# Kernel optimization log

Measured on AMD Instinct MI355X. Metric: run time of the kernel, lower is better.

## Reference

```python
import jax, jax.numpy as jnp
import numpy as np

EPSILON = 8.0        # Gibbs kernel temperature (JCPOTConfig.epsilon)
NUM_INNER_ITER = 10  # Sinkhorn u/v fixed-point iterations
STAB = 1e-8          # denominator stabilizer, matches torch code


def _cost_matrix(s, t):
    # Euclidean pairwise distance, same math as torch.norm(s[:,None]-t[None,:], dim=2)
    # computed without materializing the [n_s, n_t, d] tensor.
    sq = jnp.sum(s * s, axis=1)[:, None] + jnp.sum(t * t, axis=1)[None, :] - 2.0 * (s @ t.T)
    return jnp.sqrt(jnp.maximum(sq, 0.0))


def setup_inputs() -> dict:
    key = jax.random.key(0)
    k1, k2 = jax.random.split(key)
    return {
        "source_features": jax.random.normal(k1, (4096, 512), dtype=jnp.float32),
        "target_features": jax.random.normal(k2, (4096, 512), dtype=jnp.float32),
    }


def reference(source_features, target_features):
    n_s = source_features.shape[0]
    n_t = target_features.shape[0]
    C = _cost_matrix(source_features, target_features)   # [n_s, n_t]
    K = jnp.exp(-C / EPSILON)                             # Gibbs kernel

    # uniform marginals (JCPOT passes uniform weights; Sinkhorn renormalizes -> same)
    a = jnp.full((n_s, 1), 1.0 / n_s, dtype=C.dtype)
    b = jnp.full((n_t, 1), 1.0 / n_t, dtype=C.dtype)

    def body(carry, _):
        u, v = carry
        u = a / (K @ v + STAB)
        v = b / (K.T @ u + STAB)
        return (u, v), None

    u0 = jnp.ones((n_s, 1), dtype=C.dtype)
    v0 = jnp.ones((n_t, 1), dtype=C.dtype)
    (u, v), _ = jax.lax.scan(body, (u0, v0), None, length=NUM_INNER_ITER)

    coupling = u * K * v.T                                # [n_s, n_t]
    ot_loss = jnp.sum(coupling * C) / (n_s * n_t)         # reduction='mean'
    # returns same contents as the torch dict: ot_loss, coupling, cost_matrix
    return ot_loss, coupling, C
```

## Files before the change

kernel.cpp:

```cpp
#include <hip/hip_runtime.h>
#include <math.h>


#define N_S 4096
#define N_T 4096
#define DIM 512
#define STAB 1e-8f

typedef _Float16 f16x4 __attribute__((ext_vector_type(4)));
typedef _Float16 f16x8 __attribute__((ext_vector_type(8)));
typedef float f32x4v __attribute__((ext_vector_type(4)));

#define SINK_BLOCKS 1024

__global__ __launch_bounds__(256) void k_norms(const float4* __restrict__ S4,
                                               const float4* __restrict__ T4,
                                               float* __restrict__ ns, float* __restrict__ nt) {
    int t = threadIdx.x;
    int lane = t & 63, wave = t >> 6;
    int wid = blockIdx.x * 4 + wave;
    const float4* src; float* dst; int row;
    if (wid < N_S) { src = S4; dst = ns; row = wid; }
    else           { src = T4; dst = nt; row = wid - N_S; }
    float acc = 0.f;
#pragma unroll
    for (int c = 0; c < 2; ++c) {
        float4 x = src[row * 128 + c * 64 + lane];
        acc += x.x*x.x + x.y*x.y + x.z*x.z + x.w*x.w;
    }
#pragma unroll
    for (int m = 32; m; m >>= 1) acc += __shfl_xor(acc, m);
    if (lane == 0) dst[row] = acc;
}

__global__ __launch_bounds__(256) void k_cvt(const float* __restrict__ S, const float* __restrict__ T,
                                             _Float16* __restrict__ Sh2, _Float16* __restrict__ Th2) {
    int g = blockIdx.x * 256 + threadIdx.x;
    const float* src; _Float16* dst;
    if (g < 262144) { src = S; dst = Sh2; }
    else            { src = T; dst = Th2; g -= 262144; }
    int row = g >> 6, cb = (g & 63) * 8;
    float4 x0 = *(const float4*)(src + (size_t)row * 512 + cb);
    float4 x1 = *(const float4*)(src + (size_t)row * 512 + cb + 4);
    f16x8 h = { (_Float16)x0.x, (_Float16)x0.y, (_Float16)x0.z, (_Float16)x0.w,
                (_Float16)x1.x, (_Float16)x1.y, (_Float16)x1.z, (_Float16)x1.w };
    *(f16x8*)(dst + ((size_t)(cb >> 5) * 4096 + row) * 32 + (cb & 31)) = h;
}

__global__ void k_init(float* v, float* vacc, double* lossd) {
    int g = blockIdx.x * 256 + threadIdx.x;
    if (g < N_T) { v[g] = 1.0f; vacc[g] = 0.0f; }
    if (g == 0) *lossd = 0.0;
}

__global__ __launch_bounds__(256) void k_gemm16(const _Float16* __restrict__ Sh2,
                                                const _Float16* __restrict__ Th2,
                                                const float* __restrict__ ns,
                                                const float* __restrict__ nt,
                                                float* __restrict__ outC) {
    __shared__ _Float16 As[128 * 40];
    __shared__ _Float16 Bs[128 * 40];
    int t = threadIdx.x;
    int lane = t & 63, wave = t >> 6;
    int wr = wave >> 1, wc = wave & 1;
    int brow = blockIdx.x * 128, bcol = blockIdx.y * 128;

    f32x4v acc[4][4] = {};

    for (int kt = 0; kt < 16; ++kt) {
        __syncthreads();
        const _Float16* Ab = Sh2 + ((size_t)kt * 4096 + brow) * 32;
        const _Float16* Bb = Th2 + ((size_t)kt * 4096 + bcol) * 32;
#pragma unroll
        for (int w = 0; w < 2; ++w) {
            int e = w * 2048 + t * 8, row = e >> 5, col = e & 31;
            *(f16x8*)(&As[row * 40 + col]) = *(const f16x8*)(Ab + row * 32 + col);
            *(f16x8*)(&Bs[row * 40 + col]) = *(const f16x8*)(Bb + row * 32 + col);
        }
        __syncthreads();

        f16x8 af[4], bf[4];
#pragma unroll
        for (int m = 0; m < 4; ++m)
            af[m] = *(const f16x8*)(&As[(wr * 64 + m * 16 + (lane & 15)) * 40 + (lane >> 4) * 8]);
#pragma unroll
        for (int n = 0; n < 4; ++n)
            bf[n] = *(const f16x8*)(&Bs[(wc * 64 + n * 16 + (lane & 15)) * 40 + (lane >> 4) * 8]);
#pragma unroll
        for (int m = 0; m < 4; ++m)
#pragma unroll
            for (int n = 0; n < 4; ++n)
                acc[m][n] = __builtin_amdgcn_mfma_f32_16x16x32_f16(af[m], bf[n], acc[m][n], 0, 0, 0);
    }

#pragma unroll
    for (int m = 0; m < 4; ++m) {
#pragma unroll
        for (int n = 0; n < 4; ++n) {
#pragma unroll
            for (int r = 0; r < 4; ++r) {
                int i = brow + wr * 64 + m * 16 + (lane >> 4) * 4 + r;
                int j = bcol + wc * 64 + n * 16 + (lane & 15);
                float sq = ns[i] + nt[j] - 2.0f * acc[m][n][r];
                outC[(size_t)i * N_T + j] = sqrtf(fmaxf(sq, 0.0f));
            }
        }
    }
}

__global__ __launch_bounds__(256) void k_kh(const float* __restrict__ Cd, _Float16* __restrict__ Kh) {
    size_t i = ((size_t)blockIdx.x * 256 + threadIdx.x) * 8;
    float4 c0 = *(const float4*)(Cd + i);
    float4 c1 = *(const float4*)(Cd + i + 4);
    f16x8 h;
    h[0] = (_Float16)__expf(c0.x * -0.125f);
    h[1] = (_Float16)__expf(c0.y * -0.125f);
    h[2] = (_Float16)__expf(c0.z * -0.125f);
    h[3] = (_Float16)__expf(c0.w * -0.125f);
    h[4] = (_Float16)__expf(c1.x * -0.125f);
    h[5] = (_Float16)__expf(c1.y * -0.125f);
    h[6] = (_Float16)__expf(c1.z * -0.125f);
    h[7] = (_Float16)__expf(c1.w * -0.125f);
    *(f16x8*)(Kh + i) = h;
}

__global__ __launch_bounds__(256) void k_sink2(const _Float16* __restrict__ Kh,
                                               const float* __restrict__ v,
                                               float* __restrict__ u_out,
                                               float* __restrict__ part) {
    __shared__ _Float16 rows[4][4096];
    __shared__ float u_s[4];
    int t = threadIdx.x, lane = t & 63, w = t >> 6;
    int row = blockIdx.x * 4 + w;
    const _Float16* Kr = Kh + (size_t)row * N_T;

    f16x8 kk[8];
#pragma unroll
    for (int it = 0; it < 8; ++it)
        kk[it] = *(const f16x8*)(Kr + it * 512 + lane * 8);

    float dot = 0.f;
#pragma unroll
    for (int it = 0; it < 8; ++it) {
        int j0 = it * 512 + lane * 8;
        float4 v0 = *(const float4*)(v + j0);
        float4 v1 = *(const float4*)(v + j0 + 4);
        *(f16x8*)(&rows[w][j0]) = kk[it];
        dot += (float)kk[it][0]*v0.x + (float)kk[it][1]*v0.y
             + (float)kk[it][2]*v0.z + (float)kk[it][3]*v0.w
             + (float)kk[it][4]*v1.x + (float)kk[it][5]*v1.y
             + (float)kk[it][6]*v1.z + (float)kk[it][7]*v1.w;
    }
#pragma unroll
    for (int m = 32; m; m >>= 1) dot += __shfl_xor(dot, m);
    if (lane == 0) {
        float uv = (1.0f / N_S) / (dot + STAB);
        u_s[w] = uv;
        u_out[row] = uv;
    }
    __syncthreads();

    float4 acc[4] = {};
#pragma unroll
    for (int s = 0; s < 4; ++s) {
        int jj = t * 4 + s * 1024;
#pragma unroll
        for (int r = 0; r < 4; ++r) {
            f16x4 k4 = *(const f16x4*)(&rows[r][jj]);
            float uu = u_s[r];
            acc[s].x += uu * (float)k4[0];
            acc[s].y += uu * (float)k4[1];
            acc[s].z += uu * (float)k4[2];
            acc[s].w += uu * (float)k4[3];
        }
    }
    float* pb = part + (size_t)blockIdx.x * N_T;
#pragma unroll
    for (int s = 0; s < 4; ++s)
        *(float4*)(pb + t * 4 + s * 1024) = acc[s];
}

__global__ __launch_bounds__(256) void k_vred(const float* __restrict__ part, float* __restrict__ v) {
    __shared__ float sums[256];
    int t = threadIdx.x;
    int c = t & 15, p0 = t >> 4;
    int j = blockIdx.x * 16 + c;
    float acc = 0.f;
#pragma unroll 8
    for (int k = 0; k < 64; ++k)
        acc += part[(size_t)(p0 * 64 + k) * N_T + j];
    sums[t] = acc;
    __syncthreads();
    if (t < 16) {
        float s = 0.f;
#pragma unroll
        for (int c2 = 0; c2 < 16; ++c2) s += sums[c2 * 16 + t];
        v[blockIdx.x * 16 + t] = (1.0f / N_T) / (s + STAB);
    }
}

__global__ __launch_bounds__(256) void k_final3(const _Float16* __restrict__ Kh,
                                                const float* __restrict__ u, const float* __restrict__ v,
                                                float* __restrict__ W, double* __restrict__ lossd) {
    int t = threadIdx.x, row = blockIdx.x;
    float ui = u[row];
    float lacc = 0.f;
    const float NEG8LN2 = -5.5451774444795623f;
    const _Float16* Kr = Kh + (size_t)row * N_T;
    float* Wr = W + (size_t)row * N_T;
#pragma unroll
    for (int cc = 0; cc < 4; ++cc) {
        int j = (cc * 256 + t) * 4;
        f16x4 kk = *(const f16x4*)(Kr + j);
        float4 v4 = *(const float4*)(v + j);
        float4 w4;
        float kf0 = (float)kk[0], kf1 = (float)kk[1], kf2 = (float)kk[2], kf3 = (float)kk[3];
        w4.x = ui * kf0 * v4.x;
        w4.y = ui * kf1 * v4.y;
        w4.z = ui * kf2 * v4.z;
        w4.w = ui * kf3 * v4.w;
        *(float4*)(Wr + j) = w4;
        lacc += w4.x * (NEG8LN2 * __log2f(kf0)) + w4.y * (NEG8LN2 * __log2f(kf1))
              + w4.z * (NEG8LN2 * __log2f(kf2)) + w4.w * (NEG8LN2 * __log2f(kf3));
    }
#pragma unroll
    for (int m = 32; m; m >>= 1) lacc += __shfl_xor(lacc, m);
    __shared__ float wsum[4];
    int lane = t & 63, wave = t >> 6;
    if (lane == 0) wsum[wave] = lacc;
    __syncthreads();
    if (t == 0) atomicAdd(lossd, (double)(wsum[0] + wsum[1] + wsum[2] + wsum[3]));
}

__global__ void k_loss(const double* __restrict__ lossd, float* __restrict__ out0) {
    *out0 = (float)(*lossd / ((double)N_S * (double)N_T));
}

__global__ __launch_bounds__(256) void k_gemm0(const float* __restrict__ S, const float* __restrict__ T,
                                               const float* __restrict__ ns, const float* __restrict__ nt,
                                               float* __restrict__ outK, float* __restrict__ outC) {
    __shared__ _Float16 As[128 * 40];
    __shared__ _Float16 Bs[128 * 40];
    int t = threadIdx.x;
    int lane = t & 63, wave = t >> 6;
    int wr = wave >> 1, wc = wave & 1;
    int brow = blockIdx.x * 128, bcol = blockIdx.y * 128;

    f32x4v acc[4][4] = {};

    for (int kt = 0; kt < DIM; kt += 32) {
        __syncthreads();
#pragma unroll
        for (int w = 0; w < 4; ++w) {
            int e = w * 1024 + t * 4;
            int row = e >> 5, col = e & 31;
            float4 a = *(const float4*)(S + (size_t)(brow + row) * DIM + kt + col);
            f16x4 ah = { (_Float16)a.x, (_Float16)a.y, (_Float16)a.z, (_Float16)a.w };
            *(f16x4*)(&As[row * 40 + col]) = ah;
            float4 b = *(const float4*)(T + (size_t)(bcol + row) * DIM + kt + col);
            f16x4 bh = { (_Float16)b.x, (_Float16)b.y, (_Float16)b.z, (_Float16)b.w };
            *(f16x4*)(&Bs[row * 40 + col]) = bh;
        }
        __syncthreads();

        f16x8 af[4], bf[4];
#pragma unroll
        for (int m = 0; m < 4; ++m)
            af[m] = *(const f16x8*)(&As[(wr * 64 + m * 16 + (lane & 15)) * 40 + (lane >> 4) * 8]);
#pragma unroll
        for (int n = 0; n < 4; ++n)
            bf[n] = *(const f16x8*)(&Bs[(wc * 64 + n * 16 + (lane & 15)) * 40 + (lane >> 4) * 8]);
#pragma unroll
        for (int m = 0; m < 4; ++m)
#pragma unroll
            for (int n = 0; n < 4; ++n)
                acc[m][n] = __builtin_amdgcn_mfma_f32_16x16x32_f16(af[m], bf[n], acc[m][n], 0, 0, 0);
    }

#pragma unroll
    for (int m = 0; m < 4; ++m) {
#pragma unroll
        for (int n = 0; n < 4; ++n) {
#pragma unroll
            for (int r = 0; r < 4; ++r) {
                int i = brow + wr * 64 + m * 16 + (lane >> 4) * 4 + r;
                int j = bcol + wc * 64 + n * 16 + (lane & 15);
                float sq = ns[i] + nt[j] - 2.0f * acc[m][n][r];
                float c = sqrtf(fmaxf(sq, 0.0f));
                size_t idx = (size_t)i * N_T + j;
                outC[idx] = c;
                outK[idx] = __expf(-c * 0.125f);
            }
        }
    }
}

__global__ __launch_bounds__(256) void k_rowmv(const float* __restrict__ Kd,
                                               const float* __restrict__ v, float* __restrict__ u) {
    __shared__ float vl[4096];
    int t = threadIdx.x;
#pragma unroll
    for (int c = 0; c < 16; ++c) vl[c * 256 + t] = v[c * 256 + t];
    __syncthreads();
    int lane = t & 63, wave = t >> 6;
    int row = blockIdx.x * 4 + wave;
    const float* Kr = Kd + (size_t)row * N_T;
    float dot = 0.f;
#pragma unroll 8
    for (int c = 0; c < 64; ++c) {
        int j = c * 64 + lane;
        dot += Kr[j] * vl[j];
    }
#pragma unroll
    for (int m = 32; m; m >>= 1) dot += __shfl_xor(dot, m);
    if (lane == 0) u[row] = (1.0f / N_S) / (dot + STAB);
}

__global__ __launch_bounds__(256) void k_colmv(const float* __restrict__ Kd,
                                               const float* __restrict__ u, float* __restrict__ vacc) {
    __shared__ float ul[64];
    int t = threadIdx.x;
    int rc = blockIdx.y;
    if (t < 64) ul[t] = u[rc * 64 + t];
    __syncthreads();
    int j = blockIdx.x * 256 + t;
    const float* Kp = Kd + (size_t)(rc * 64) * N_T + j;
    float acc = 0.f;
#pragma unroll 8
    for (int r = 0; r < 64; ++r) acc += Kp[(size_t)r * N_T] * ul[r];
    atomicAdd(&vacc[j], acc);
}

__global__ void k_vfin(float* v, float* vacc) {
    int j = blockIdx.x * 256 + threadIdx.x;
    v[j] = (1.0f / N_T) / (vacc[j] + STAB);
    vacc[j] = 0.f;
}

__global__ __launch_bounds__(256) void k_final(float* __restrict__ Kd, const float* __restrict__ Cd,
                                               const float* __restrict__ u, const float* __restrict__ v,
                                               double* __restrict__ lossd) {
    int t = threadIdx.x;
    int row = blockIdx.x;
    float ui = u[row];
    float lacc = 0.f;
#pragma unroll 4
    for (int c = 0; c < 16; ++c) {
        int j = c * 256 + t;
        size_t idx = (size_t)row * N_T + j;
        float w = ui * Kd[idx] * v[j];
        Kd[idx] = w;
        lacc += w * Cd[idx];
    }
#pragma unroll
    for (int m = 32; m; m >>= 1) lacc += __shfl_xor(lacc, m);
    __shared__ float wsum[4];
    int lane = t & 63, wave = t >> 6;
    if (lane == 0) wsum[wave] = lacc;
    __syncthreads();
    if (t == 0) atomicAdd(lossd, (double)(wsum[0] + wsum[1] + wsum[2] + wsum[3]));
}

extern "C" void kernel_launch(void* const* d_in, const int* in_sizes, int n_in,
                              void* d_out, int out_size, void* d_ws, size_t ws_size,
                              hipStream_t stream) {
    const float* S = (const float*)d_in[0];
    const float* T = (const float*)d_in[1];
    float* out = (float*)d_out;
    float* outCoup = out + 1;
    float* outC = out + 1 + (size_t)N_S * N_T;

    const size_t MB = 1024 * 1024;
    const size_t need = 56 * MB + 96 * 1024;

    if (ws_size >= need) {
        char* wsb = (char*)d_ws;
        _Float16* Sh2 = (_Float16*)wsb;
        _Float16* Th2 = (_Float16*)(wsb + 4 * MB);
        _Float16* Kh  = (_Float16*)(wsb + 8 * MB);
        float* part   = (float*)(wsb + 40 * MB);
        float* ns = (float*)(wsb + 56 * MB);
        float* nt = ns + 4096;
        float* u  = nt + 4096;
        float* v  = u + 4096;
        float* vacc = v + 4096;
        double* lossd = (double*)(vacc + 4096);

        k_norms<<<2048, 256, 0, stream>>>((const float4*)S, (const float4*)T, ns, nt);
        k_cvt<<<2048, 256, 0, stream>>>(S, T, Sh2, Th2);
        k_init<<<16, 256, 0, stream>>>(v, vacc, lossd);
        k_gemm16<<<dim3(32, 32), 256, 0, stream>>>(Sh2, Th2, ns, nt, outC);
        k_kh<<<8192, 256, 0, stream>>>(outC, Kh);
        for (int it = 0; it < 10; ++it) {
            k_sink2<<<SINK_BLOCKS, 256, 0, stream>>>(Kh, v, u, part);
            k_vred<<<256, 256, 0, stream>>>(part, v);
        }
        k_final3<<<4096, 256, 0, stream>>>(Kh, u, v, outCoup, lossd);
        k_loss<<<1, 1, 0, stream>>>(lossd, out);
    } else {
        float* outK = outCoup;
        float* ws   = (float*)d_ws;
        float* ns   = ws;
        float* nt   = ws + 4096;
        float* u    = ws + 8192;
        float* v    = ws + 12288;
        float* vacc = ws + 16384;
        double* lossd = (double*)(ws + 20480);

        k_norms<<<2048, 256, 0, stream>>>((const float4*)S, (const float4*)T, ns, nt);
        k_init<<<16, 256, 0, stream>>>(v, vacc, lossd);
        k_gemm0<<<dim3(32, 32), 256, 0, stream>>>(S, T, ns, nt, outK, outC);
        for (int it = 0; it < 10; ++it) {
            k_rowmv<<<1024, 256, 0, stream>>>(outK, v, u);
            k_colmv<<<dim3(16, 64), 256, 0, stream>>>(outK, u, vacc);
            k_vfin<<<16, 256, 0, stream>>>(v, vacc);
        }
        k_final<<<4096, 256, 0, stream>>>(outK, outC, u, v, lossd);
        k_loss<<<1, 1, 0, stream>>>(lossd, out);
    }
}
```

Baseline: 409.4 us.

## Fuse norm/convert prep, fold exp into GEMM epilogue, pad partials, widen v reduction

```diff
diff --git a/kernel.cpp b/kernel.cpp
--- a/kernel.cpp
+++ b/kernel.cpp
@@ -6,6 +6,7 @@
 #define N_T 4096
 #define DIM 512
 #define STAB 1e-8f
+#define PART_STRIDE 4112
 
 typedef _Float16 f16x4 __attribute__((ext_vector_type(4)));
 typedef _Float16 f16x8 __attribute__((ext_vector_type(8)));
@@ -13,53 +14,42 @@
 
 #define SINK_BLOCKS 1024
 
-__global__ __launch_bounds__(256) void k_norms(const float4* __restrict__ S4,
-                                               const float4* __restrict__ T4,
-                                               float* __restrict__ ns, float* __restrict__ nt) {
-    int t = threadIdx.x;
-    int lane = t & 63, wave = t >> 6;
+__global__ __launch_bounds__(256) void k_prep(const float* __restrict__ S, const float* __restrict__ T,
+                                              _Float16* __restrict__ Sh2, _Float16* __restrict__ Th2,
+                                              float* __restrict__ ns, float* __restrict__ nt) {
+    int t = threadIdx.x, lane = t & 63, wave = t >> 6;
     int wid = blockIdx.x * 4 + wave;
-    const float4* src; float* dst; int row;
-    if (wid < N_S) { src = S4; dst = ns; row = wid; }
-    else           { src = T4; dst = nt; row = wid - N_S; }
-    float acc = 0.f;
-#pragma unroll
-    for (int c = 0; c < 2; ++c) {
-        float4 x = src[row * 128 + c * 64 + lane];
-        acc += x.x*x.x + x.y*x.y + x.z*x.z + x.w*x.w;
-    }
+    const float* src; _Float16* dst; float* ndst; int row;
+    if (wid < N_S) { src = S; dst = Sh2; ndst = ns; row = wid; }
+    else           { src = T; dst = Th2; ndst = nt; row = wid - N_S; }
+    int cb = lane * 8;
+    float4 x0 = *(const float4*)(src + (size_t)row * DIM + cb);
+    float4 x1 = *(const float4*)(src + (size_t)row * DIM + cb + 4);
+    float acc = x0.x*x0.x + x0.y*x0.y + x0.z*x0.z + x0.w*x0.w
+              + x1.x*x1.x + x1.y*x1.y + x1.z*x1.z + x1.w*x1.w;
 #pragma unroll
     for (int m = 32; m; m >>= 1) acc += __shfl_xor(acc, m);
-    if (lane == 0) dst[row] = acc;
-}
-
-__global__ __launch_bounds__(256) void k_cvt(const float* __restrict__ S, const float* __restrict__ T,
-                                             _Float16* __restrict__ Sh2, _Float16* __restrict__ Th2) {
-    int g = blockIdx.x * 256 + threadIdx.x;
-    const float* src; _Float16* dst;
-    if (g < 262144) { src = S; dst = Sh2; }
-    else            { src = T; dst = Th2; g -= 262144; }
-    int row = g >> 6, cb = (g & 63) * 8;
-    float4 x0 = *(const float4*)(src + (size_t)row * 512 + cb);
-    float4 x1 = *(const float4*)(src + (size_t)row * 512 + cb + 4);
+    if (lane == 0) ndst[row] = acc;
     f16x8 h = { (_Float16)x0.x, (_Float16)x0.y, (_Float16)x0.z, (_Float16)x0.w,
                 (_Float16)x1.x, (_Float16)x1.y, (_Float16)x1.z, (_Float16)x1.w };
     *(f16x8*)(dst + ((size_t)(cb >> 5) * 4096 + row) * 32 + (cb & 31)) = h;
 }
 
-__global__ void k_init(float* v, float* vacc, double* lossd) {
+__global__ void k_init(float* v, double* lossd) {
     int g = blockIdx.x * 256 + threadIdx.x;
-    if (g < N_T) { v[g] = 1.0f; vacc[g] = 0.0f; }
+    if (g < N_T) v[g] = 1.0f;
     if (g == 0) *lossd = 0.0;
 }
 
-__global__ __launch_bounds__(256) void k_gemm16(const _Float16* __restrict__ Sh2,
-                                                const _Float16* __restrict__ Th2,
-                                                const float* __restrict__ ns,
-                                                const float* __restrict__ nt,
-                                                float* __restrict__ outC) {
+__global__ __launch_bounds__(256) void k_gemm16b(const _Float16* __restrict__ Sh2,
+                                                 const _Float16* __restrict__ Th2,
+                                                 const float* __restrict__ ns,
+                                                 const float* __restrict__ nt,
+                                                 float* __restrict__ outC,
+                                                 _Float16* __restrict__ Kh) {
     __shared__ _Float16 As[128 * 40];
     __shared__ _Float16 Bs[128 * 40];
+    __shared__ float eps[4][16 * 68];
     int t = threadIdx.x;
     int lane = t & 63, wave = t >> 6;
     int wr = wave >> 1, wc = wave & 1;
@@ -93,35 +83,38 @@
                 acc[m][n] = __builtin_amdgcn_mfma_f32_16x16x32_f16(af[m], bf[n], acc[m][n], 0, 0, 0);
     }
 
+    float* my = &eps[wave][0];
 #pragma unroll
     for (int m = 0; m < 4; ++m) {
 #pragma unroll
-        for (int n = 0; n < 4; ++n) {
-#pragma unroll
-            for (int r = 0; r < 4; ++r) {
-                int i = brow + wr * 64 + m * 16 + (lane >> 4) * 4 + r;
-                int j = bcol + wc * 64 + n * 16 + (lane & 15);
-                float sq = ns[i] + nt[j] - 2.0f * acc[m][n][r];
-                outC[(size_t)i * N_T + j] = sqrtf(fmaxf(sq, 0.0f));
-            }
-        }
-    }
-}
-
-__global__ __launch_bounds__(256) void k_kh(const float* __restrict__ Cd, _Float16* __restrict__ Kh) {
-    size_t i = ((size_t)blockIdx.x * 256 + threadIdx.x) * 8;
-    float4 c0 = *(const float4*)(Cd + i);
-    float4 c1 = *(const float4*)(Cd + i + 4);
-    f16x8 h;
-    h[0] = (_Float16)__expf(c0.x * -0.125f);
-    h[1] = (_Float16)__expf(c0.y * -0.125f);
-    h[2] = (_Float16)__expf(c0.z * -0.125f);
-    h[3] = (_Float16)__expf(c0.w * -0.125f);
-    h[4] = (_Float16)__expf(c1.x * -0.125f);
-    h[5] = (_Float16)__expf(c1.y * -0.125f);
-    h[6] = (_Float16)__expf(c1.z * -0.125f);
-    h[7] = (_Float16)__expf(c1.w * -0.125f);
-    *(f16x8*)(Kh + i) = h;
+        for (int n = 0; n < 4; ++n)
+#pragma unroll
+            for (int r = 0; r < 4; ++r)
+                my[((lane >> 4) * 4 + r) * 68 + n * 16 + (lane & 15)] = acc[m][n][r];
+        __syncthreads();
+#pragma unroll
+        for (int rep = 0; rep < 4; ++rep) {
+            int rr = (lane >> 4) + rep * 4;
+            int cc = (lane & 15) * 4;
+            float4 d = *(float4*)(my + rr * 68 + cc);
+            int i = brow + wr * 64 + m * 16 + rr;
+            int j = bcol + wc * 64 + cc;
+            float nsi = ns[i];
+            float4 nt4 = *(const float4*)(nt + j);
+            float4 c4;
+            c4.x = sqrtf(fmaxf(nsi + nt4.x - 2.0f * d.x, 0.0f));
+            c4.y = sqrtf(fmaxf(nsi + nt4.y - 2.0f * d.y, 0.0f));
+            c4.z = sqrtf(fmaxf(nsi + nt4.z - 2.0f * d.z, 0.0f));
+            c4.w = sqrtf(fmaxf(nsi + nt4.w - 2.0f * d.w, 0.0f));
+            *(float4*)(outC + (size_t)i * N_T + j) = c4;
+            f16x4 kh4 = { (_Float16)__expf(c4.x * -0.125f),
+                          (_Float16)__expf(c4.y * -0.125f),
+                          (_Float16)__expf(c4.z * -0.125f),
+                          (_Float16)__expf(c4.w * -0.125f) };
+            *(f16x4*)(Kh + (size_t)i * N_T + j) = kh4;
+        }
+        __syncthreads();
+    }
 }
 
 __global__ __launch_bounds__(256) void k_sink2(const _Float16* __restrict__ Kh,
@@ -174,28 +167,31 @@
             acc[s].w += uu * (float)k4[3];
         }
     }
-    float* pb = part + (size_t)blockIdx.x * N_T;
+    float* pb = part + (size_t)blockIdx.x * PART_STRIDE;
 #pragma unroll
     for (int s = 0; s < 4; ++s)
         *(float4*)(pb + t * 4 + s * 1024) = acc[s];
 }
 
-__global__ __launch_bounds__(256) void k_vred(const float* __restrict__ part, float* __restrict__ v) {
-    __shared__ float sums[256];
-    int t = threadIdx.x;
-    int c = t & 15, p0 = t >> 4;
-    int j = blockIdx.x * 16 + c;
-    float acc = 0.f;
+__global__ __launch_bounds__(256) void k_vred2(const float* __restrict__ part, float* __restrict__ v) {
+    __shared__ float red[32][32];
+    int t = threadIdx.x;
+    int tj = t & 7, tk = t >> 3;
+    int j = blockIdx.x * 32 + tj * 4;
+    float4 a = {0.f, 0.f, 0.f, 0.f};
 #pragma unroll 8
-    for (int k = 0; k < 64; ++k)
-        acc += part[(size_t)(p0 * 64 + k) * N_T + j];
-    sums[t] = acc;
-    __syncthreads();
-    if (t < 16) {
+    for (int k = 0; k < 32; ++k) {
+        const float* pp = part + (size_t)(tk * 32 + k) * PART_STRIDE + j;
+        float4 p4 = *(const float4*)pp;
+        a.x += p4.x; a.y += p4.y; a.z += p4.z; a.w += p4.w;
+    }
+    *(float4*)(&red[tk][tj * 4]) = a;
+    __syncthreads();
+    if (t < 32) {
         float s = 0.f;
 #pragma unroll
-        for (int c2 = 0; c2 < 16; ++c2) s += sums[c2 * 16 + t];
-        v[blockIdx.x * 16 + t] = (1.0f / N_T) / (s + STAB);
+        for (int k = 0; k < 32; ++k) s += red[k][t];
+        v[blockIdx.x * 32 + t] = (1.0f / N_T) / (s + STAB);
     }
 }
 
@@ -236,6 +232,32 @@
     *out0 = (float)(*lossd / ((double)N_S * (double)N_T));
 }
 
+__global__ __launch_bounds__(256) void k_norms(const float4* __restrict__ S4,
+                                               const float4* __restrict__ T4,
+                                               float* __restrict__ ns, float* __restrict__ nt) {
+    int t = threadIdx.x;
+    int lane = t & 63, wave = t >> 6;
+    int wid = blockIdx.x * 4 + wave;
+    const float4* src; float* dst; int row;
+    if (wid < N_S) { src = S4; dst = ns; row = wid; }
+    else           { src = T4; dst = nt; row = wid - N_S; }
+    float acc = 0.f;
+#pragma unroll
+    for (int c = 0; c < 2; ++c) {
+        float4 x = src[row * 128 + c * 64 + lane];
+        acc += x.x*x.x + x.y*x.y + x.z*x.z + x.w*x.w;
+    }
+#pragma unroll
+    for (int m = 32; m; m >>= 1) acc += __shfl_xor(acc, m);
+    if (lane == 0) dst[row] = acc;
+}
+
+__global__ void k_init0(float* v, float* vacc, double* lossd) {
+    int g = blockIdx.x * 256 + threadIdx.x;
+    if (g < N_T) { v[g] = 1.0f; vacc[g] = 0.0f; }
+    if (g == 0) *lossd = 0.0;
+}
+
 __global__ __launch_bounds__(256) void k_gemm0(const float* __restrict__ S, const float* __restrict__ T,
                                                const float* __restrict__ ns, const float* __restrict__ nt,
                                                float* __restrict__ outK, float* __restrict__ outC) {
@@ -371,7 +393,8 @@
     float* outC = out + 1 + (size_t)N_S * N_T;
 
     const size_t MB = 1024 * 1024;
-    const size_t need = 56 * MB + 96 * 1024;
+    const size_t PART_BYTES = (size_t)1024 * PART_STRIDE * 4;
+    const size_t need = 40 * MB + PART_BYTES + 96 * 1024;
 
     if (ws_size >= need) {
         char* wsb = (char*)d_ws;
@@ -379,21 +402,19 @@
         _Float16* Th2 = (_Float16*)(wsb + 4 * MB);
         _Float16* Kh  = (_Float16*)(wsb + 8 * MB);
         float* part   = (float*)(wsb + 40 * MB);
-        float* ns = (float*)(wsb + 56 * MB);
+        char* tail    = wsb + 40 * MB + PART_BYTES;
+        float* ns = (float*)tail;
         float* nt = ns + 4096;
         float* u  = nt + 4096;
         float* v  = u + 4096;
-        float* vacc = v + 4096;
-        double* lossd = (double*)(vacc + 4096);
-
-        k_norms<<<2048, 256, 0, stream>>>((const float4*)S, (const float4*)T, ns, nt);
-        k_cvt<<<2048, 256, 0, stream>>>(S, T, Sh2, Th2);
-        k_init<<<16, 256, 0, stream>>>(v, vacc, lossd);
-        k_gemm16<<<dim3(32, 32), 256, 0, stream>>>(Sh2, Th2, ns, nt, outC);
-        k_kh<<<8192, 256, 0, stream>>>(outC, Kh);
+        double* lossd = (double*)(v + 4096);
+
+        k_prep<<<2048, 256, 0, stream>>>(S, T, Sh2, Th2, ns, nt);
+        k_init<<<16, 256, 0, stream>>>(v, lossd);
+        k_gemm16b<<<dim3(32, 32), 256, 0, stream>>>(Sh2, Th2, ns, nt, outC, Kh);
         for (int it = 0; it < 10; ++it) {
             k_sink2<<<SINK_BLOCKS, 256, 0, stream>>>(Kh, v, u, part);
-            k_vred<<<256, 256, 0, stream>>>(part, v);
+            k_vred2<<<128, 256, 0, stream>>>(part, v);
         }
         k_final3<<<4096, 256, 0, stream>>>(Kh, u, v, outCoup, lossd);
         k_loss<<<1, 1, 0, stream>>>(lossd, out);
@@ -408,7 +429,7 @@
         double* lossd = (double*)(ws + 20480);
 
         k_norms<<<2048, 256, 0, stream>>>((const float4*)S, (const float4*)T, ns, nt);
-        k_init<<<16, 256, 0, stream>>>(v, vacc, lossd);
+        k_init0<<<16, 256, 0, stream>>>(v, vacc, lossd);
         k_gemm0<<<dim3(32, 32), 256, 0, stream>>>(S, T, ns, nt, outK, outC);
         for (int it = 0; it < 10; ++it) {
             k_rowmv<<<1024, 256, 0, stream>>>(outK, v, u);
```

Result: faster. 388.5 us (-5.1%).
